# Optimization experiments

Measured on AMD Instinct MI355X. Metric: run time of the kernel, lower is better.

Reference implementation:

```python
import jax, jax.numpy as jnp
import numpy as np

H = 128      # hidden_channels
G = 512      # number of graphs in the batch
NEG_SLOPE = 0.2


def _seg_sum(x, idx, n):
    return jax.ops.segment_sum(x, idx, num_segments=n)


def _sage(x_src, x_dst, ei, Wl, bl, Wr):
    # PyG SAGEConv: lin_l(mean_j x_j) + lin_r(x_i); lin_l has bias, lin_r does not.
    s, d = ei[0], ei[1]
    n = x_dst.shape[0]
    agg = _seg_sum(x_src[s], d, n)
    cnt = _seg_sum(jnp.ones((ei.shape[1],), x_src.dtype), d, n)
    mean = agg / jnp.maximum(cnt, 1.0)[:, None]
    return mean @ Wl + bl + x_dst @ Wr


def _gat(x_src, x_dst, ei, Ws, Wd, a_s, a_d, b):
    # PyG GATConv (heads=1, add_self_loops=False, bipartite): segment softmax over dst.
    s, d = ei[0], ei[1]
    n = x_dst.shape[0]
    hs = x_src @ Ws                                  # [N_src, H]
    hd = x_dst @ Wd                                  # [N_dst, H]
    logit = jax.nn.leaky_relu((hs @ a_s)[s] + (hd @ a_d)[d], NEG_SLOPE)
    m = jax.ops.segment_max(logit, d, num_segments=n)
    e = jnp.exp(logit - m[d])
    z = _seg_sum(e, d, n)
    alpha = e / jnp.maximum(z[d], 1e-16)
    return _seg_sum(alpha[:, None] * hs[s], d, n) + b


def _gcn(x, ei, W, b):
    # PyG GCNConv with add_self_loops=True, normalize=True (same src/dst node type).
    s, d = ei[0], ei[1]
    n = x.shape[0]
    deg = _seg_sum(jnp.ones((ei.shape[1],), x.dtype), d, n) + 1.0  # +1 self loop
    dis = jax.lax.rsqrt(deg)
    h = x @ W
    norm = dis[s] * dis[d]
    out = _seg_sum(norm[:, None] * h[s], d, n) + (dis * dis)[:, None] * h
    return out + b


def _pool(x, b):
    s = _seg_sum(x, b, G)
    c = _seg_sum(jnp.ones((x.shape[0],), x.dtype), b, G)
    return s / jnp.maximum(c, 1.0)[:, None]


def setup_inputs() -> dict:
    key = jax.random.key(0)
    ks = iter(jax.random.split(key, 80))
    scale = 1.0 / np.sqrt(H)

    def nrm(shape, sc=scale):
        return jax.random.normal(next(ks), shape, jnp.float32) * sc

    def edges(e, n_src, n_dst):
        src = jax.random.randint(next(ks), (e,), 0, n_src, jnp.int32)
        dst = jax.random.randint(next(ks), (e,), 0, n_dst, jnp.int32)
        return jnp.stack([src, dst])

    def batch(n):
        return jnp.sort(jax.random.randint(next(ks), (n,), 0, G, jnp.int32))

    N_CD, N_SEQ, N_ANNO, N_RANGE, N_MD = 100000, 80000, 80000, 80000, 50000
    inp = {
        'x_cd': nrm((N_CD, H), 1.0), 'x_seq': nrm((N_SEQ, H), 1.0),
        'x_anno': nrm((N_ANNO, H), 1.0), 'x_range': nrm((N_RANGE, H), 1.0),
        'x_md': nrm((N_MD, H), 1.0),
        'ei_seq': edges(160000, N_CD, N_SEQ),
        'ei_anno': edges(200000, N_CD, N_ANNO),
        'ei_range': edges(200000, N_CD, N_RANGE),
        'ei_comp': edges(300000, N_MD, N_CD),
        'ei_cc': edges(300000, N_CD, N_CD),
        'ei_mm': edges(150000, N_MD, N_MD),
        'b_cd': batch(N_CD), 'b_seq': batch(N_SEQ), 'b_anno': batch(N_ANNO),
        'b_range': batch(N_RANGE), 'b_md': batch(N_MD),
    }
    # per-layer stacked params (leading axis = 2 layers)
    for nm, shp in [('Wsl_seq', (2, H, H)), ('bs_seq', (2, H)), ('Wsr_seq', (2, H, H)),
                    ('Wsl_anno', (2, H, H)), ('bs_anno', (2, H)), ('Wsr_anno', (2, H, H)),
                    ('Wg_comp_s', (2, H, H)), ('Wg_comp_d', (2, H, H)),
                    ('ag_comp_s', (2, H)), ('ag_comp_d', (2, H)), ('bg_comp', (2, H)),
                    ('Wg_range_s', (2, H, H)), ('Wg_range_d', (2, H, H)),
                    ('ag_range_s', (2, H)), ('ag_range_d', (2, H)), ('bg_range', (2, H)),
                    ('Wc_cc', (2, H, H)), ('bc_cc', (2, H)),
                    ('Wc_mm', (2, H, H)), ('bc_mm', (2, H)),
                    ('lin1_W', (5 * H, H)), ('lin1_b', (H,)),
                    ('lin2_W', (H, 1)), ('lin2_b', (1,))]:
        inp[nm] = nrm(shp)
    return inp


def reference(x_cd, x_seq, x_anno, x_range, x_md,
              ei_seq, ei_anno, ei_range, ei_comp, ei_cc, ei_mm,
              b_cd, b_seq, b_anno, b_range, b_md,
              Wsl_seq, bs_seq, Wsr_seq, Wsl_anno, bs_anno, Wsr_anno,
              Wg_comp_s, Wg_comp_d, ag_comp_s, ag_comp_d, bg_comp,
              Wg_range_s, Wg_range_d, ag_range_s, ag_range_d, bg_range,
              Wc_cc, bc_cc, Wc_mm, bc_mm,
              lin1_W, lin1_b, lin2_W, lin2_b):
    for l in range(2):
        # HeteroConv aggr='sum': CD receives GAT(MD->CD) + GCN(CD->CD)
        n_cd = (_gat(x_md, x_cd, ei_comp, Wg_comp_s[l], Wg_comp_d[l],
                     ag_comp_s[l], ag_comp_d[l], bg_comp[l])
                + _gcn(x_cd, ei_cc, Wc_cc[l], bc_cc[l]))
        n_seq = _sage(x_cd, x_seq, ei_seq, Wsl_seq[l], bs_seq[l], Wsr_seq[l])
        n_anno = _sage(x_cd, x_anno, ei_anno, Wsl_anno[l], bs_anno[l], Wsr_anno[l])
        n_range = _gat(x_cd, x_range, ei_range, Wg_range_s[l], Wg_range_d[l],
                       ag_range_s[l], ag_range_d[l], bg_range[l])
        n_md = _gcn(x_md, ei_mm, Wc_mm[l], bc_mm[l])
        x_cd, x_seq, x_anno, x_range, x_md = (
            jax.nn.relu(n_cd), jax.nn.relu(n_seq), jax.nn.relu(n_anno),
            jax.nn.relu(n_range), jax.nn.relu(n_md))
    emb = jnp.concatenate([_pool(x_cd, b_cd), _pool(x_seq, b_seq),
                           _pool(x_anno, b_anno), _pool(x_range, b_range),
                           _pool(x_md, b_md)], axis=-1)        # [G, 5H]
    h = jax.nn.relu(emb @ lin1_W + lin1_b)  # Dropout(0.7) is identity in eval
    return (h @ lin2_W + lin2_b).reshape(-1)  # [G]
```

## Files before the change

### kernel.cpp

```cpp
#include <hip/hip_runtime.h>

#define HD 128
#define GNUM 512
#define RPB 520
#define IDXCAP 512
#define TM 32

typedef __attribute__((ext_vector_type(8))) short short8v;
typedef __attribute__((ext_vector_type(4))) float f32x4;

__device__ __forceinline__ void split1(float a, short& h, short& l) {
  unsigned u = __float_as_uint(a);
  unsigned hb = (u + 0x7FFFu + ((u >> 16) & 1u)) & 0xFFFF0000u;
  h = (short)(hb >> 16);
  float rest = a - __uint_as_float(hb);
  unsigned u2 = __float_as_uint(rest);
  l = (short)((u2 + 0x7FFFu + ((u2 >> 16) & 1u)) >> 16);
}

struct WTab { const float* p[8]; };
__global__ __launch_bounds__(256) void k_split_w(WTab tab, short* __restrict__ whi,
                                                 short* __restrict__ wlo)
{
  int m = blockIdx.x >> 6;
  int i = (blockIdx.x & 63) * 256 + threadIdx.x;
  const float* W = tab.p[m >> 1] + (m & 1) * 16384;
  int k = i >> 7, n = i & 127;
  short h, l;
  split1(W[k * 128 + n], h, l);
  whi[m * 16384 + n * 128 + k] = h;
  wlo[m * 16384 + n * 128 + k] = l;
}

#define CF_LD 132
__global__ __launch_bounds__(256) void k_gemm_mfma(
    const float* __restrict__ A1, const short* __restrict__ WH1, const short* __restrict__ WL1,
    const int* __restrict__ grp, const int* __restrict__ gcol,
    const float* __restrict__ A2, const short* __restrict__ WH2, const short* __restrict__ WL2,
    float* __restrict__ C, const float* __restrict__ bias, int N, int relu,
    const float* __restrict__ avec, float* __restrict__ adot)
{
  __shared__ char smem[TM * 136 * 2 * 2];
  __shared__ int idxbuf[IDXCAP];
  short* Ah = (short*)smem;
  short* Al = Ah + TM * 136;
  float* Cf = (float*)smem;

  const int t = threadIdx.x;
  const int row0 = blockIdx.x * TM;
  const int lane = t & 63, wid = t >> 6;
  const int g = lane >> 4, cn = lane & 15;
  const int colbase = wid * 32;

  f32x4 zero = {0.f, 0.f, 0.f, 0.f};
  f32x4 acc[2][2];
#pragma unroll
  for (int rt = 0; rt < 2; ++rt) { acc[rt][0] = zero; acc[rt][1] = zero; }

  auto stageA = [&](const float* __restrict__ A) {
    const float4* A4 = (const float4*)(A + (size_t)row0 * 128);
#pragma unroll
    for (int i = 0; i < 4; ++i) {
      int f4 = t + i * 256;
      int row = f4 >> 5, c4 = f4 & 31;
      float4 v = make_float4(0.f, 0.f, 0.f, 0.f);
      if (row0 + row < N) v = A4[f4];
      short4 h, l;
      split1(v.x, h.x, l.x); split1(v.y, h.y, l.y);
      split1(v.z, h.z, l.z); split1(v.w, h.w, l.w);
      *(short4*)(Ah + row * 136 + c4 * 4) = h;
      *(short4*)(Al + row * 136 + c4 * 4) = l;
    }
  };

  auto stageA_gather = [&](const float* __restrict__ X, int e_lo) {
#pragma unroll
    for (int i = 0; i < 4; ++i) {
      int f4 = t + i * 256;
      int row = f4 >> 5, ln = f4 & 31;
      int r = row0 + row;
      float4 s = make_float4(0.f, 0.f, 0.f, 0.f);
      int e0 = 0, e1 = 0;
      if (r < N) { e0 = grp[r]; e1 = grp[r + 1]; }
      int e = e0;
      for (; e + 1 < e1; e += 2) {
        int off0 = e - e_lo, off1 = off0 + 1;
        int c0 = (off0 < IDXCAP) ? idxbuf[off0] : gcol[e];
        int c1 = (off1 < IDXCAP) ? idxbuf[off1] : gcol[e + 1];
        float4 v0 = *(const float4*)(X + (size_t)c0 * 128 + ln * 4);
        float4 v1 = *(const float4*)(X + (size_t)c1 * 128 + ln * 4);
        s.x += v0.x + v1.x; s.y += v0.y + v1.y;
        s.z += v0.z + v1.z; s.w += v0.w + v1.w;
      }
      if (e < e1) {
        int off = e - e_lo;
        int c = (off < IDXCAP) ? idxbuf[off] : gcol[e];
        float4 v = *(const float4*)(X + (size_t)c * 128 + ln * 4);
        s.x += v.x; s.y += v.y; s.z += v.z; s.w += v.w;
      }
      float inv = 1.f / fmaxf((float)(e1 - e0), 1.f);
      short4 h, l;
      split1(s.x * inv, h.x, l.x); split1(s.y * inv, h.y, l.y);
      split1(s.z * inv, h.z, l.z); split1(s.w * inv, h.w, l.w);
      *(short4*)(Ah + row * 136 + ln * 4) = h;
      *(short4*)(Al + row * 136 + ln * 4) = l;
    }
  };

  auto accum = [&](const short* __restrict__ WH, const short* __restrict__ WL) {
#pragma unroll
    for (int kg = 0; kg < 4; ++kg) {
      short8v bhi[2], blo[2];
#pragma unroll
      for (int ct = 0; ct < 2; ++ct) {
        size_t o = (size_t)(colbase + ct * 16 + cn) * 128 + kg * 32 + g * 8;
        bhi[ct] = *(const short8v*)(WH + o);
        blo[ct] = *(const short8v*)(WL + o);
      }
#pragma unroll
      for (int rt = 0; rt < 2; ++rt) {
        const int ao = (rt * 16 + cn) * 136 + kg * 32 + g * 8;
        const short8v ah = *(const short8v*)(Ah + ao);
        const short8v al = *(const short8v*)(Al + ao);
#pragma unroll
        for (int ct = 0; ct < 2; ++ct) {
          acc[rt][ct] = __builtin_amdgcn_mfma_f32_16x16x32_bf16(ah, bhi[ct], acc[rt][ct], 0, 0, 0);
          acc[rt][ct] = __builtin_amdgcn_mfma_f32_16x16x32_bf16(al, bhi[ct], acc[rt][ct], 0, 0, 0);
          acc[rt][ct] = __builtin_amdgcn_mfma_f32_16x16x32_bf16(ah, blo[ct], acc[rt][ct], 0, 0, 0);
        }
      }
    }
  };

  if (grp) {
    const int row_end = min(row0 + TM, N);
    const int e_lo = grp[row0];
    const int cnt = min(grp[row_end] - e_lo, IDXCAP);
    for (int k = t; k < cnt; k += 256) idxbuf[k] = gcol[e_lo + k];
    __syncthreads();
    stageA_gather(A1, e_lo);
  } else {
    stageA(A1);
  }
  __syncthreads();
  accum(WH1, WL1);
  if (A2) {
    __syncthreads();
    stageA(A2);
    __syncthreads();
    accum(WH2, WL2);
  }
  __syncthreads();

  if (avec) {
    float* part = (float*)smem;
    const float av0 = avec[colbase + cn];
    const float av1 = avec[colbase + 16 + cn];
#pragma unroll
    for (int rt = 0; rt < 2; ++rt)
#pragma unroll
      for (int r = 0; r < 4; ++r) {
        float p = fmaf(acc[rt][1][r], av1, acc[rt][0][r] * av0);
#pragma unroll
        for (int o = 1; o < 16; o <<= 1) p += __shfl_xor(p, o);
        if (cn == 0) part[wid * TM + rt * 16 + g * 4 + r] = p;
      }
    __syncthreads();
    if (t < TM) {
      int row = row0 + t;
      if (row < N) adot[row] = part[t] + part[TM + t] + part[2 * TM + t] + part[3 * TM + t];
    }
    __syncthreads();
  }

#pragma unroll
  for (int rt = 0; rt < 2; ++rt)
#pragma unroll
    for (int ct = 0; ct < 2; ++ct)
#pragma unroll
      for (int r = 0; r < 4; ++r)
        Cf[(rt * 16 + g * 4 + r) * CF_LD + colbase + ct * 16 + cn] = acc[rt][ct][r];
  __syncthreads();

  float4* C4 = (float4*)(C + (size_t)row0 * 128);
#pragma unroll
  for (int i = 0; i < 4; ++i) {
    int f4 = t + i * 256;
    int row = f4 >> 5, c4 = f4 & 31;
    if (row0 + row < N) {
      float4 v = *(const float4*)(Cf + row * CF_LD + c4 * 4);
      if (bias) {
        float4 bv = *(const float4*)(bias + c4 * 4);
        v.x += bv.x; v.y += bv.y; v.z += bv.z; v.w += bv.w;
      }
      if (relu) {
        v.x = fmaxf(v.x, 0.f); v.y = fmaxf(v.y, 0.f);
        v.z = fmaxf(v.z, 0.f); v.w = fmaxf(v.w, 0.f);
      }
      C4[f4] = v;
    }
  }
}

__global__ void k_rowdot(const float* __restrict__ x, const float* __restrict__ a,
                         float* __restrict__ out, int N)
{
  int wid = blockIdx.x * 4 + (threadIdx.x >> 6);
  int lane = threadIdx.x & 63;
  if (wid >= N) return;
  float2 xv = ((const float2*)x)[(size_t)wid * 64 + lane];
  float2 av = ((const float2*)a)[lane];
  float v = fmaf(xv.y, av.y, xv.x * av.x);
#pragma unroll
  for (int o = 32; o > 0; o >>= 1) v += __shfl_down(v, o);
  if (lane == 0) out[wid] = v;
}

struct MTab { const float* W[4]; const float* a[4]; };
__global__ __launch_bounds__(128) void k_matvec4(MTab tb, float* __restrict__ wv)
{
  __shared__ float as[128];
  int m = blockIdx.x, i = threadIdx.x;
  as[i] = tb.a[m][i];
  __syncthreads();
  const float* W = tb.W[m];
  float v = 0.f;
  for (int j = 0; j < 128; ++j) v = fmaf(W[i * 128 + j], as[j], v);
  wv[m * 128 + i] = v;
}

struct HTab { const int* key[6]; int* cnt[6]; unsigned short* rank[6]; int bo[7]; int n[6]; };
__global__ void k_hist_rank_all(HTab tb) {
  int bi = blockIdx.x, ty = 0;
  while (ty < 5 && bi >= tb.bo[ty + 1]) ++ty;
  int i = (bi - tb.bo[ty]) * 256 + threadIdx.x;
  if (i < tb.n[ty])
    tb.rank[ty][i] = (unsigned short)atomicAdd(&tb.cnt[ty][tb.key[ty][i]], 1);
}

struct FTab { const int* es[6]; const int* ed[6]; const int* rp[6];
              const unsigned short* rank[6]; int* col[6]; int bo[7]; int n[6]; };
__global__ void k_fill_all(FTab tb) {
  int bi = blockIdx.x, ty = 0;
  while (ty < 5 && bi >= tb.bo[ty + 1]) ++ty;
  int e = (bi - tb.bo[ty]) * 256 + threadIdx.x;
  if (e >= tb.n[ty]) return;
  int p = tb.rp[ty][tb.ed[ty][e]] + (int)tb.rank[ty][e];
  tb.col[ty][p] = tb.es[ty][e];
}

struct STab { int* rp[6]; int* bs[6]; int n[6]; int bo[7]; };

__global__ __launch_bounds__(256) void k_scan_partial_all(STab tb) {
  __shared__ int red[256];
  int bi = blockIdx.x, ty = 0;
  while (ty < 5 && bi >= tb.bo[ty + 1]) ++ty;
  int lb = bi - tb.bo[ty];
  const int* rp = tb.rp[ty];
  const int N = tb.n[ty];
  const int t = threadIdx.x, base = lb * 4096;
  int s = 0;
  for (int i = t; i < 4096; i += 256) {
    int idx = base + i;
    if (idx < N) s += rp[idx];
  }
  red[t] = s;
  __syncthreads();
  for (int ofs = 128; ofs > 0; ofs >>= 1) {
    if (t < ofs) red[t] += red[t + ofs];
    __syncthreads();
  }
  if (t == 0) tb.bs[ty][lb] = red[0];
}

__global__ __launch_bounds__(256) void k_scan_bsums_all(STab tb) {
  __shared__ int sh[256];
  const int ty = blockIdx.x;
  const int nb = (tb.n[ty] + 4095) / 4096;
  const int t = threadIdx.x;
  int v = (t < nb) ? tb.bs[ty][t] : 0;
  sh[t] = v;
  __syncthreads();
  for (int ofs = 1; ofs < 256; ofs <<= 1) {
    int u = (t >= ofs) ? sh[t - ofs] : 0;
    __syncthreads();
    sh[t] += u;
    __syncthreads();
  }
  if (t < nb) tb.bs[ty][t] = sh[t] - v;
  if (t == 255) tb.rp[ty][tb.n[ty]] = sh[255];
}

__global__ __launch_bounds__(256) void k_scan_final_all(STab tb) {
  __shared__ int sh[4096 + 256];
  __shared__ int tsum[256];
  int bi = blockIdx.x, ty = 0;
  while (ty < 5 && bi >= tb.bo[ty + 1]) ++ty;
  int lb = bi - tb.bo[ty];
  int* rp = tb.rp[ty];
  const int N = tb.n[ty];
  const int t = threadIdx.x, base = lb * 4096;
  auto mp = [](int i) { return i + (i >> 4); };
#pragma unroll
  for (int i = 0; i < 16; ++i) {
    int idx = base + i * 256 + t;
    sh[mp(i * 256 + t)] = (idx < N) ? rp[idx] : 0;
  }
  __syncthreads();
  int s = 0;
#pragma unroll
  for (int j = 0; j < 16; ++j) s += sh[mp(t * 16 + j)];
  tsum[t] = s;
  __syncthreads();
  for (int ofs = 1; ofs < 256; ofs <<= 1) {
    int u = (t >= ofs) ? tsum[t - ofs] : 0;
    __syncthreads();
    tsum[t] += u;
    __syncthreads();
  }
  int pre = tsum[t] - s + tb.bs[ty][lb];
#pragma unroll
  for (int j = 0; j < 16; ++j) {
    int v = sh[mp(t * 16 + j)];
    sh[mp(t * 16 + j)] = pre;
    pre += v;
  }
  __syncthreads();
#pragma unroll
  for (int i = 0; i < 16; ++i) {
    int idx = base + i * 256 + t;
    if (idx < N) rp[idx] = sh[mp(i * 256 + t)];
  }
}

struct BTab { const int* b[5]; int n[5]; };
__global__ __launch_bounds__(512) void k_runptr(BTab tb, int* __restrict__ rpb_all) {
  const int ty = blockIdx.x;
  const int* b = tb.b[ty];
  const int N = tb.n[ty];
  const int t = threadIdx.x;
  int lo = 0, hi = N;
  while (lo < hi) {
    int mid = (lo + hi) >> 1;
    if (b[mid] < t) lo = mid + 1; else hi = mid;
  }
  rpb_all[ty * RPB + t] = lo;
  if (t == 0) rpb_all[ty * RPB + GNUM] = N;
}

struct DTab { const int* rp[2]; float* dis[2]; int n[2]; int bo[3]; };
__global__ void k_dis2(DTab tb) {
  int bi = blockIdx.x, ty = (bi >= tb.bo[1]) ? 1 : 0;
  int n = (bi - tb.bo[ty]) * 256 + threadIdx.x;
  if (n < tb.n[ty]) tb.dis[ty][n] = rsqrtf((float)(tb.rp[ty][n + 1] - tb.rp[ty][n]) + 1.f);
}

__global__ void k_gcn_gather(const int* __restrict__ rp, const int* __restrict__ col,
                             const float* __restrict__ dis, const float* __restrict__ h,
                             const float* addin, const float* __restrict__ b,
                             float* out, int N,
                             const float* __restrict__ dvec, float* __restrict__ dout)
{
  int node = blockIdx.x * 4 + (threadIdx.x >> 6);
  if (node >= N) return;
  int lane = threadIdx.x & 63;
  int s0 = rp[node], deg = rp[node + 1] - s0;
  float rd = dis[node];
  const float2* h2 = (const float2*)h;
  float2 hself = h2[(size_t)node * 64 + lane];
  float2 bv = ((const float2*)b)[lane];
  float ad0 = 0.f, ad1 = 0.f;
  if (addin) {
    float2 a2 = ((const float2*)addin)[(size_t)node * 64 + lane];
    ad0 = a2.x; ad1 = a2.y;
  }
  float a0 = 0.f, a1 = 0.f, b0 = 0.f, b1 = 0.f;
  for (int base = 0; base < deg; base += 64) {
    int m = min(64, deg - base);
    int c = 0; float dv = 0.f;
    if (lane < m) { c = col[s0 + base + lane]; dv = dis[c]; }
    int j = 0;
    for (; j + 1 < m; j += 2) {
      int sA = __shfl(c, j), sB = __shfl(c, j + 1);
      float nA = __shfl(dv, j) * rd, nB = __shfl(dv, j + 1) * rd;
      float2 vA = h2[(size_t)sA * 64 + lane];
      float2 vB = h2[(size_t)sB * 64 + lane];
      a0 = fmaf(nA, vA.x, a0); a1 = fmaf(nA, vA.y, a1);
      b0 = fmaf(nB, vB.x, b0); b1 = fmaf(nB, vB.y, b1);
    }
    if (j < m) {
      int sA = __shfl(c, j);
      float nA = __shfl(dv, j) * rd;
      float2 vA = h2[(size_t)sA * 64 + lane];
      a0 = fmaf(nA, vA.x, a0); a1 = fmaf(nA, vA.y, a1);
    }
  }
  float rr = rd * rd;
  float v0 = fmaf(rr, hself.x, a0 + b0) + bv.x + ad0;
  float v1 = fmaf(rr, hself.y, a1 + b1) + bv.y + ad1;
  v0 = fmaxf(v0, 0.f); v1 = fmaxf(v1, 0.f);
  ((float2*)out)[(size_t)node * 64 + lane] = make_float2(v0, v1);
  if (dvec) {
    float2 wv = ((const float2*)dvec)[lane];
    float p = fmaf(v1, wv.y, v0 * wv.x);
#pragma unroll
    for (int o = 32; o > 0; o >>= 1) p += __shfl_xor(p, o);
    if (lane == 0) dout[node] = p;
  }
}

__global__ void k_gat_gather(const int* __restrict__ rp, const int* __restrict__ col,
                             const float* __restrict__ hs, const float* __restrict__ as_,
                             const float* __restrict__ ad_, const float* __restrict__ b,
                             float* __restrict__ out, int N, int relu,
                             const float* __restrict__ dvec, float* __restrict__ dout)
{
  int node = blockIdx.x * 4 + (threadIdx.x >> 6);
  if (node >= N) return;
  int lane = threadIdx.x & 63;
  int s0 = rp[node], deg = rp[node + 1] - s0;
  float adn = ad_[node];
  float2 bv = ((const float2*)b)[lane];
  const float2* hs2 = (const float2*)hs;
  float z = 0.f, a0 = 0.f, a1 = 0.f, b0 = 0.f, b1 = 0.f;
  for (int base = 0; base < deg; base += 64) {
    int m = min(64, deg - base);
    int c = 0; float av = 0.f;
    if (lane < m) { c = col[s0 + base + lane]; av = as_[c]; }
    int j = 0;
    for (; j + 1 < m; j += 2) {
      int sA = __shfl(c, j), sB = __shfl(c, j + 1);
      float vA = __shfl(av, j) + adn, vB = __shfl(av, j + 1) + adn;
      vA = vA > 0.f ? vA : 0.2f * vA;
      vB = vB > 0.f ? vB : 0.2f * vB;
      float pA = __expf(vA), pB = __expf(vB);
      z += pA + pB;
      float2 hA = hs2[(size_t)sA * 64 + lane];
      float2 hB = hs2[(size_t)sB * 64 + lane];
      a0 = fmaf(pA, hA.x, a0); a1 = fmaf(pA, hA.y, a1);
      b0 = fmaf(pB, hB.x, b0); b1 = fmaf(pB, hB.y, b1);
    }
    if (j < m) {
      int sA = __shfl(c, j);
      float vA = __shfl(av, j) + adn;
      vA = vA > 0.f ? vA : 0.2f * vA;
      float pA = __expf(vA);
      z += pA;
      float2 hA = hs2[(size_t)sA * 64 + lane];
      a0 = fmaf(pA, hA.x, a0); a1 = fmaf(pA, hA.y, a1);
    }
  }
  float inv = (deg > 0) ? 1.f / z : 0.f;
  float v0 = fmaf(a0 + b0, inv, bv.x);
  float v1 = fmaf(a1 + b1, inv, bv.y);
  if (relu) { v0 = fmaxf(v0, 0.f); v1 = fmaxf(v1, 0.f); }
  ((float2*)out)[(size_t)node * 64 + lane] = make_float2(v0, v1);
  if (dvec) {
    float2 wv = ((const float2*)dvec)[lane];
    float p = fmaf(v1, wv.y, v0 * wv.x);
#pragma unroll
    for (int o = 32; o > 0; o >>= 1) p += __shfl_xor(p, o);
    if (lane == 0) dout[node] = p;
  }
}

__global__ __launch_bounds__(256) void k_pool_seg(
    const float* __restrict__ x, const int* __restrict__ rpb,
    float* __restrict__ pool, int col_off)
{
  __shared__ float2 red2[4][64];
  const int g = blockIdx.x;
  const int t = threadIdx.x, w = t >> 6, lane = t & 63;
  const int n0 = rpb[g], n1 = rpb[g + 1];
  const float2* x2 = (const float2*)x;
  float a0 = 0.f, a1 = 0.f, b0 = 0.f, b1 = 0.f;
  int n = n0 + w;
  for (; n + 4 < n1; n += 8) {
    float2 vA = x2[(size_t)n * 64 + lane];
    float2 vB = x2[(size_t)(n + 4) * 64 + lane];
    a0 += vA.x; a1 += vA.y; b0 += vB.x; b1 += vB.y;
  }
  if (n < n1) { float2 vA = x2[(size_t)n * 64 + lane]; a0 += vA.x; a1 += vA.y; }
  red2[w][lane] = make_float2(a0 + b0, a1 + b1);
  __syncthreads();
  if (t < 64) {
    float2 r0 = red2[0][t], r1 = red2[1][t], r2 = red2[2][t], r3 = red2[3][t];
    float inv = 1.f / fmaxf((float)(n1 - n0), 1.f);
    ((float2*)(pool + (size_t)g * 640 + col_off))[t] =
        make_float2((r0.x + r1.x + r2.x + r3.x) * inv,
                    (r0.y + r1.y + r2.y + r3.y) * inv);
  }
}

__global__ void k_mlp(const float* __restrict__ pool,
                      const float* __restrict__ W1, const float* __restrict__ b1,
                      const float* __restrict__ W2, const float* __restrict__ b2,
                      float* __restrict__ out)
{
  __shared__ float emb[640];
  __shared__ float red[128];
  const int g = blockIdx.x, t = threadIdx.x;
  for (int i = t; i < 640; i += 128) emb[i] = pool[(size_t)g * 640 + i];
  __syncthreads();
  float acc = b1[t];
  for (int i = 0; i < 640; ++i) acc = fmaf(emb[i], W1[i * 128 + t], acc);
  float h = fmaxf(acc, 0.f);
  red[t] = h * W2[t];
  __syncthreads();
  for (int s = 64; s > 0; s >>= 1) {
    if (t < s) red[t] += red[t + s];
    __syncthreads();
  }
  if (t == 0) out[g] = red[0] + b2[0];
}

extern "C" void kernel_launch(void* const* d_in, const int* in_sizes, int n_in,
                              void* d_out, int out_size, void* d_ws, size_t ws_size,
                              hipStream_t stream)
{
  auto fin = [&](int i) { return (const float*)d_in[i]; };
  auto iin = [&](int i) { return (const int*)d_in[i]; };

  const float *x_cd = fin(0), *x_seq = fin(1), *x_anno = fin(2), *x_range = fin(3), *x_md = fin(4);
  const int *ei_seq = iin(5), *ei_anno = iin(6), *ei_range = iin(7),
            *ei_comp = iin(8), *ei_cc = iin(9), *ei_mm = iin(10);
  const int *b_cd = iin(11), *b_seq = iin(12), *b_anno = iin(13), *b_range = iin(14), *b_md = iin(15);

  const int N_CD = in_sizes[0] / HD, N_SEQ = in_sizes[1] / HD, N_ANNO = in_sizes[2] / HD,
            N_RANGE = in_sizes[3] / HD, N_MD = in_sizes[4] / HD;
  const int E_seq = in_sizes[5] / 2, E_anno = in_sizes[6] / 2, E_range = in_sizes[7] / 2,
            E_comp = in_sizes[8] / 2, E_cc = in_sizes[9] / 2, E_mm = in_sizes[10] / 2;
  const int N_OTH = max(max(N_SEQ, N_ANNO), N_RANGE);

  auto WLm = [&](int i, int l) { return fin(i) + (size_t)l * HD * HD; };
  auto WLv = [&](int i, int l) { return fin(i) + (size_t)l * HD; };

  float* ws = (float*)d_ws;
  size_t off = 0;
  auto alloc = [&](size_t n) { float* p = ws + off; off += (n + 3) & ~(size_t)3; return p; };
  float* xcd1 = alloc((size_t)N_CD * HD);
  float* xmd1 = alloc((size_t)N_MD * HD);
  float* xoth = alloc((size_t)N_OTH * HD);
  float* acc  = alloc((size_t)N_CD * HD);
  float* t1   = alloc((size_t)N_CD * HD);
  float* sAs  = alloc((size_t)N_CD);
  float* sAd  = alloc((size_t)N_CD);
  float* sAd2 = alloc((size_t)N_CD);
  float* dis_cc = alloc((size_t)N_CD);
  float* dis_mm = alloc((size_t)N_MD);
  float* wvall = alloc(4 * HD);
  float* pool = alloc((size_t)GNUM * 5 * HD);
  short* whi = (short*)(ws + off); off += (size_t)16 * 16384 / 2;
  short* wlo = (short*)(ws + off); off += (size_t)16 * 16384 / 2;
  auto alloci = [&](size_t n) { int* p = (int*)(ws + off); off += (n + 3) & ~(size_t)3; return p; };
  int* bsall = alloci(6 * 256);
  int* rpb_all = alloci(5 * RPB);
  int Nds[6] = {N_SEQ, N_ANNO, N_RANGE, N_CD, N_CD, N_MD};
  int Es[6]  = {E_seq, E_anno, E_range, E_comp, E_cc, E_mm};
  int* rps[6];
  int* rp0 = alloci(0);
  { size_t tot = 0; for (int i = 0; i < 6; ++i) tot += (size_t)Nds[i] + 1;
    int* p = alloci(tot); rp0 = p;
    for (int i = 0; i < 6; ++i) { rps[i] = p; p += Nds[i] + 1; } }
  size_t rp_tot_bytes = 0; for (int i = 0; i < 6; ++i) rp_tot_bytes += ((size_t)Nds[i] + 1) * 4;
  unsigned short* ranks[6];
  for (int i = 0; i < 6; ++i) ranks[i] = (unsigned short*)alloci(((size_t)Es[i] + 1) / 2);
  int* cols[6];  for (int i = 0; i < 6; ++i) cols[i] = alloci((size_t)Es[i]);
  (void)n_in;

  if (off * sizeof(float) > ws_size) {
    hipMemsetAsync(d_out, 0, (size_t)out_size * sizeof(float), stream);
    return;
  }

  auto ew = [&](size_t elems) { return dim3((unsigned)((elems + 255) / 256)); };
  auto nw = [&](int N) { return dim3((unsigned)((N + 3) / 4)); };

  WTab tab;
  tab.p[0] = fin(16); tab.p[1] = fin(18); tab.p[2] = fin(19); tab.p[3] = fin(21);
  tab.p[4] = fin(22); tab.p[5] = fin(27); tab.p[6] = fin(32); tab.p[7] = fin(34);
  k_split_w<<<dim3(1024), dim3(256), 0, stream>>>(tab, whi, wlo);

  MTab mt;
  mt.W[0] = WLm(23, 0); mt.a[0] = WLv(25, 0);
  mt.W[1] = WLm(23, 1); mt.a[1] = WLv(25, 1);
  mt.W[2] = WLm(28, 0); mt.a[2] = WLv(30, 0);
  mt.W[3] = WLm(28, 1); mt.a[3] = WLv(30, 1);
  k_matvec4<<<dim3(4), dim3(128), 0, stream>>>(mt, wvall);

  {
    BTab bt;
    bt.b[0] = b_cd; bt.n[0] = N_CD;  bt.b[1] = b_seq; bt.n[1] = N_SEQ;
    bt.b[2] = b_anno; bt.n[2] = N_ANNO;  bt.b[3] = b_range; bt.n[3] = N_RANGE;
    bt.b[4] = b_md; bt.n[4] = N_MD;
    k_runptr<<<dim3(5), dim3(512), 0, stream>>>(bt, rpb_all);
  }

  const int* ess[6] = {ei_seq, ei_anno, ei_range, ei_comp, ei_cc, ei_mm};
  const int* eds[6] = {ei_seq + E_seq, ei_anno + E_anno, ei_range + E_range,
                       ei_comp + E_comp, ei_cc + E_cc, ei_mm + E_mm};
  hipMemsetAsync(rp0, 0, rp_tot_bytes, stream);
  {
    HTab ht; int b = 0;
    for (int i = 0; i < 6; ++i) {
      ht.key[i] = eds[i]; ht.cnt[i] = rps[i]; ht.rank[i] = ranks[i];
      ht.bo[i] = b; b += (Es[i] + 255) / 256; ht.n[i] = Es[i];
    }
    ht.bo[6] = b;
    k_hist_rank_all<<<dim3(b), dim3(256), 0, stream>>>(ht);
  }
  {
    STab st; int b = 0;
    for (int i = 0; i < 6; ++i) {
      st.rp[i] = rps[i]; st.bs[i] = bsall + i * 256;
      st.n[i] = Nds[i]; st.bo[i] = b; b += (Nds[i] + 4095) / 4096;
    }
    st.bo[6] = b;
    k_scan_partial_all<<<dim3(b), dim3(256), 0, stream>>>(st);
    k_scan_bsums_all<<<dim3(6), dim3(256), 0, stream>>>(st);
    k_scan_final_all<<<dim3(b), dim3(256), 0, stream>>>(st);
  }
  {
    FTab ft; int b = 0;
    for (int i = 0; i < 6; ++i) {
      ft.es[i] = ess[i]; ft.ed[i] = eds[i]; ft.rp[i] = rps[i]; ft.rank[i] = ranks[i];
      ft.col[i] = cols[i]; ft.bo[i] = b; b += (Es[i] + 255) / 256; ft.n[i] = Es[i];
    }
    ft.bo[6] = b;
    k_fill_all<<<dim3(b), dim3(256), 0, stream>>>(ft);
  }
  int *rp_seq = rps[0], *rp_anno = rps[1], *rp_range = rps[2],
      *rp_comp = rps[3], *rp_cc = rps[4], *rp_mm = rps[5];
  int *col_seq = cols[0], *col_anno = cols[1], *col_range = cols[2],
      *col_comp = cols[3], *col_cc = cols[4], *col_mm = cols[5];
  {
    DTab dt;
    dt.rp[0] = rp_cc; dt.dis[0] = dis_cc; dt.n[0] = N_CD;
    dt.rp[1] = rp_mm; dt.dis[1] = dis_mm; dt.n[1] = N_MD;
    dt.bo[0] = 0; dt.bo[1] = (N_CD + 255) / 256;
    dt.bo[2] = dt.bo[1] + (N_MD + 255) / 256;
    k_dis2<<<dim3(dt.bo[2]), dim3(256), 0, stream>>>(dt);
  }

  auto WHp = [&](int sidx, int layer) { return whi + (size_t)(sidx * 2 + layer) * 16384; };
  auto WLp = [&](int sidx, int layer) { return wlo + (size_t)(sidx * 2 + layer) * 16384; };
  auto gemm = [&](const float* A, int sidx, int layer, float* C, const float* b,
                  int N, int relu, const float* avec = nullptr, float* adot = nullptr) {
    k_gemm_mfma<<<dim3((N + TM - 1) / TM), dim3(256), 0, stream>>>(
        A, WHp(sidx, layer), WLp(sidx, layer), nullptr, nullptr,
        nullptr, nullptr, nullptr, C, b, N, relu, avec, adot);
  };
  auto gemm2g = [&](const float* xsrc, const int* grp, const int* gcol, int s1,
                    const float* xself, int s2, int layer,
                    float* C, const float* b, int N) {
    k_gemm_mfma<<<dim3((N + TM - 1) / TM), dim3(256), 0, stream>>>(
        xsrc, WHp(s1, layer), WLp(s1, layer), grp, gcol,
        xself, WHp(s2, layer), WLp(s2, layer), C, b, N, 1, nullptr, nullptr);
  };
  auto do_pool = [&](const float* x, int type) {
    k_pool_seg<<<dim3(GNUM), dim3(256), 0, stream>>>(x, rpb_all + type * RPB, pool, type * HD);
  };

  auto gat = [&](const float* xs, const float* xd, const int* rp, const int* col,
                 int Ns, int Nd, int sidx, int layer, const float* avs_raw,
                 const float* sAd_src, int wvD,
                 const float* dvec, float* dout,
                 const float* bias, float* out, int relu) {
    if (wvD >= 0) {
      k_rowdot<<<nw(Nd), dim3(256), 0, stream>>>(xd, wvall + wvD * 128, sAd, Nd);
      sAd_src = sAd;
    }
    gemm(xs, sidx, layer, t1, nullptr, Ns, 0, avs_raw, sAs);
    k_gat_gather<<<nw(Nd), dim3(256), 0, stream>>>(rp, col, t1, sAs, sAd_src, bias,
                                                   out, Nd, relu, dvec, dout);
  };
  auto gcn = [&](const float* x, const int* rp, const int* col, const float* dis, int N,
                 int sidx, int layer, const float* b, const float* addin, float* out,
                 const float* dvec, float* dout) {
    gemm(x, sidx, layer, t1, nullptr, N, 0);
    k_gcn_gather<<<nw(N), dim3(256), 0, stream>>>(rp, col, dis, t1, addin, b, out, N,
                                                  dvec, dout);
  };
  auto sage = [&](const float* xsrc, const float* xself, const int* rp, const int* col,
                  int Nd, int sl, int sr, int layer, const float* bl, float* out) {
    gemm2g(xsrc, rp, col, sl, xself, sr, layer, out, bl, Nd);
  };

  gat(x_md, x_cd, rp_comp, col_comp, N_MD, N_CD, 4, 0, WLv(24, 0),
      nullptr, 0, nullptr, nullptr, WLv(26, 0), acc, 0);
  gcn(x_cd, rp_cc, col_cc, dis_cc, N_CD, 6, 0, WLv(33, 0), acc, xcd1,
      wvall + 1 * 128, sAd2);
  gcn(x_md, rp_mm, col_mm, dis_mm, N_MD, 7, 0, WLv(35, 0), nullptr, xmd1,
      nullptr, nullptr);
  gat(xmd1, xcd1, rp_comp, col_comp, N_MD, N_CD, 4, 1, WLv(24, 1),
      sAd2, -1, nullptr, nullptr, WLv(26, 1), acc, 0);
  gcn(xcd1, rp_cc, col_cc, dis_cc, N_CD, 6, 1, WLv(33, 1), acc, acc,
      nullptr, nullptr);
  do_pool(acc, 0);
  gcn(xmd1, rp_mm, col_mm, dis_mm, N_MD, 7, 1, WLv(35, 1), nullptr, acc,
      nullptr, nullptr);
  do_pool(acc, 4);

  sage(x_cd, x_seq, rp_seq, col_seq, N_SEQ, 0, 1, 0, WLv(17, 0), xoth);
  sage(xcd1, xoth, rp_seq, col_seq, N_SEQ, 0, 1, 1, WLv(17, 1), acc);
  do_pool(acc, 1);
  sage(x_cd, x_anno, rp_anno, col_anno, N_ANNO, 2, 3, 0, WLv(20, 0), xoth);
  sage(xcd1, xoth, rp_anno, col_anno, N_ANNO, 2, 3, 1, WLv(20, 1), acc);
  do_pool(acc, 2);
  gat(x_cd, x_range, rp_range, col_range, N_CD, N_RANGE, 5, 0, WLv(29, 0),
      nullptr, 2, wvall + 3 * 128, sAd2, WLv(31, 0), xoth, 1);
  gat(xcd1, xoth, rp_range, col_range, N_CD, N_RANGE, 5, 1, WLv(29, 1),
      sAd2, -1, nullptr, nullptr, WLv(31, 1), acc, 1);
  do_pool(acc, 3);

  k_mlp<<<dim3(GNUM), dim3(128), 0, stream>>>(
      pool, fin(36), fin(37), fin(38), fin(39), (float*)d_out);
}
```

Measured before the change: 988.0 us.

## Aggregate before transform: fuse GAT/GCN gathers into the MFMA GEMM prologue

Uses linearity to aggregate neighbour features first and then multiply by the weight, so GCN and GAT become a single gather-then-GEMM kernel instead of a GEMM into a temporary followed by a separate gather kernel. Attention logits are computed up front from precomputed W·a vectors via row dots and fused epilogue dot products, removing the intermediate h matrix write/read. The cost is that gathers now read raw inputs inside the GEMM staging, where the per-row work is imbalanced. Softmax also runs without max subtraction, as it did before.

```diff
diff --git a/kernel.cpp b/kernel.cpp
--- a/kernel.cpp
+++ b/kernel.cpp
@@ -33,15 +33,19 @@
 }
 
 #define CF_LD 132
-__global__ __launch_bounds__(256) void k_gemm_mfma(
+__global__ __launch_bounds__(256) void k_gemm_conv(
     const float* __restrict__ A1, const short* __restrict__ WH1, const short* __restrict__ WL1,
-    const int* __restrict__ grp, const int* __restrict__ gcol,
+    const int* __restrict__ grp, const int* __restrict__ gcol, int mode,
+    const float* __restrict__ wsrc, const float* __restrict__ rowsc,
     const float* __restrict__ A2, const short* __restrict__ WH2, const short* __restrict__ WL2,
-    float* __restrict__ C, const float* __restrict__ bias, int N, int relu,
-    const float* __restrict__ avec, float* __restrict__ adot)
+    float* __restrict__ C, const float* __restrict__ bias, const float* addin,
+    int N, int relu,
+    const float* __restrict__ avec, float* __restrict__ adot,
+    const float* __restrict__ avec2, float* __restrict__ adot2)
 {
   __shared__ char smem[TM * 136 * 2 * 2];
   __shared__ int idxbuf[IDXCAP];
+  __shared__ float wbuf[IDXCAP];
   short* Ah = (short*)smem;
   short* Al = Ah + TM * 136;
   float* Cf = (float*)smem;
@@ -57,6 +61,14 @@
 #pragma unroll
   for (int rt = 0; rt < 2; ++rt) { acc[rt][0] = zero; acc[rt][1] = zero; }
 
+  auto storeAhl = [&](int row, int ln, float4 s) {
+    short4 h, l;
+    split1(s.x, h.x, l.x); split1(s.y, h.y, l.y);
+    split1(s.z, h.z, l.z); split1(s.w, h.w, l.w);
+    *(short4*)(Ah + row * 136 + ln * 4) = h;
+    *(short4*)(Al + row * 136 + ln * 4) = l;
+  };
+
   auto stageA = [&](const float* __restrict__ A) {
     const float4* A4 = (const float4*)(A + (size_t)row0 * 128);
 #pragma unroll
@@ -65,15 +77,17 @@
       int row = f4 >> 5, c4 = f4 & 31;
       float4 v = make_float4(0.f, 0.f, 0.f, 0.f);
       if (row0 + row < N) v = A4[f4];
-      short4 h, l;
-      split1(v.x, h.x, l.x); split1(v.y, h.y, l.y);
-      split1(v.z, h.z, l.z); split1(v.w, h.w, l.w);
-      *(short4*)(Ah + row * 136 + c4 * 4) = h;
-      *(short4*)(Al + row * 136 + c4 * 4) = l;
+      storeAhl(row, c4, v);
     }
   };
 
-  auto stageA_gather = [&](const float* __restrict__ X, int e_lo) {
+  auto getcw = [&](int e, int e_lo, int& c, float& w) {
+    int off = e - e_lo;
+    if (off < IDXCAP) { c = idxbuf[off]; w = wbuf[off]; }
+    else { c = gcol[e]; w = wsrc ? wsrc[c] : 0.f; }
+  };
+
+  auto stage_gather = [&](const float* __restrict__ X, int e_lo) {
 #pragma unroll
     for (int i = 0; i < 4; ++i) {
       int f4 = t + i * 256;
@@ -81,29 +95,54 @@
       int r = row0 + row;
       float4 s = make_float4(0.f, 0.f, 0.f, 0.f);
       int e0 = 0, e1 = 0;
-      if (r < N) { e0 = grp[r]; e1 = grp[r + 1]; }
+      float rs = 0.f;
+      if (r < N) {
+        e0 = grp[r]; e1 = grp[r + 1];
+        if (mode >= 2) rs = rowsc[r];
+      }
+      float z = 0.f;
+      if (mode == 2 && r < N) {
+        float4 xs_ = *(const float4*)(X + (size_t)r * 128 + ln * 4);
+        float rr = rs * rs;
+        s.x = rr * xs_.x; s.y = rr * xs_.y; s.z = rr * xs_.z; s.w = rr * xs_.w;
+      }
       int e = e0;
       for (; e + 1 < e1; e += 2) {
-        int off0 = e - e_lo, off1 = off0 + 1;
-        int c0 = (off0 < IDXCAP) ? idxbuf[off0] : gcol[e];
-        int c1 = (off1 < IDXCAP) ? idxbuf[off1] : gcol[e + 1];
-        float4 v0 = *(const float4*)(X + (size_t)c0 * 128 + ln * 4);
-        float4 v1 = *(const float4*)(X + (size_t)c1 * 128 + ln * 4);
-        s.x += v0.x + v1.x; s.y += v0.y + v1.y;
-        s.z += v0.z + v1.z; s.w += v0.w + v1.w;
+        int c0, c1; float w0, w1;
+        getcw(e, e_lo, c0, w0);
+        getcw(e + 1, e_lo, c1, w1);
+        float p0, p1;
+        if (mode == 3) {
+          float v0 = w0 + rs; v0 = v0 > 0.f ? v0 : 0.2f * v0;
+          float v1 = w1 + rs; v1 = v1 > 0.f ? v1 : 0.2f * v1;
+          p0 = __expf(v0); p1 = __expf(v1); z += p0 + p1;
+        } else if (mode == 2) { p0 = w0 * rs; p1 = w1 * rs; }
+        else { p0 = 1.f; p1 = 1.f; }
+        float4 a = *(const float4*)(X + (size_t)c0 * 128 + ln * 4);
+        float4 b = *(const float4*)(X + (size_t)c1 * 128 + ln * 4);
+        s.x += p0 * a.x + p1 * b.x; s.y += p0 * a.y + p1 * b.y;
+        s.z += p0 * a.z + p1 * b.z; s.w += p0 * a.w + p1 * b.w;
       }
       if (e < e1) {
-        int off = e - e_lo;
-        int c = (off < IDXCAP) ? idxbuf[off] : gcol[e];
-        float4 v = *(const float4*)(X + (size_t)c * 128 + ln * 4);
-        s.x += v.x; s.y += v.y; s.z += v.z; s.w += v.w;
-      }
-      float inv = 1.f / fmaxf((float)(e1 - e0), 1.f);
-      short4 h, l;
-      split1(s.x * inv, h.x, l.x); split1(s.y * inv, h.y, l.y);
-      split1(s.z * inv, h.z, l.z); split1(s.w * inv, h.w, l.w);
-      *(short4*)(Ah + row * 136 + ln * 4) = h;
-      *(short4*)(Al + row * 136 + ln * 4) = l;
+        int c; float w;
+        getcw(e, e_lo, c, w);
+        float p;
+        if (mode == 3) {
+          float v = w + rs; v = v > 0.f ? v : 0.2f * v;
+          p = __expf(v); z += p;
+        } else if (mode == 2) p = w * rs;
+        else p = 1.f;
+        float4 a = *(const float4*)(X + (size_t)c * 128 + ln * 4);
+        s.x += p * a.x; s.y += p * a.y; s.z += p * a.z; s.w += p * a.w;
+      }
+      if (mode == 1) {
+        float inv = 1.f / fmaxf((float)(e1 - e0), 1.f);
+        s.x *= inv; s.y *= inv; s.z *= inv; s.w *= inv;
+      } else if (mode == 3) {
+        float inv = (e1 > e0) ? 1.f / z : 0.f;
+        s.x *= inv; s.y *= inv; s.z *= inv; s.w *= inv;
+      }
+      storeAhl(row, ln, s);
     }
   };
 
@@ -132,13 +171,17 @@
     }
   };
 
-  if (grp) {
+  if (mode != 0) {
     const int row_end = min(row0 + TM, N);
     const int e_lo = grp[row0];
     const int cnt = min(grp[row_end] - e_lo, IDXCAP);
-    for (int k = t; k < cnt; k += 256) idxbuf[k] = gcol[e_lo + k];
-    __syncthreads();
-    stageA_gather(A1, e_lo);
+    for (int k = t; k < cnt; k += 256) {
+      int idx = gcol[e_lo + k];
+      idxbuf[k] = idx;
+      if (wsrc) wbuf[k] = wsrc[idx];
+    }
+    __syncthreads();
+    stage_gather(A1, e_lo);
   } else {
     stageA(A1);
   }
@@ -151,27 +194,6 @@
     accum(WH2, WL2);
   }
   __syncthreads();
-
-  if (avec) {
-    float* part = (float*)smem;
-    const float av0 = avec[colbase + cn];
-    const float av1 = avec[colbase + 16 + cn];
-#pragma unroll
-    for (int rt = 0; rt < 2; ++rt)
-#pragma unroll
-      for (int r = 0; r < 4; ++r) {
-        float p = fmaf(acc[rt][1][r], av1, acc[rt][0][r] * av0);
-#pragma unroll
-        for (int o = 1; o < 16; o <<= 1) p += __shfl_xor(p, o);
-        if (cn == 0) part[wid * TM + rt * 16 + g * 4 + r] = p;
-      }
-    __syncthreads();
-    if (t < TM) {
-      int row = row0 + t;
-      if (row < N) adot[row] = part[t] + part[TM + t] + part[2 * TM + t] + part[3 * TM + t];
-    }
-    __syncthreads();
-  }
 
 #pragma unroll
   for (int rt = 0; rt < 2; ++rt)
@@ -193,11 +215,29 @@
         float4 bv = *(const float4*)(bias + c4 * 4);
         v.x += bv.x; v.y += bv.y; v.z += bv.z; v.w += bv.w;
       }
+      if (addin) {
+        float4 av = *(const float4*)(addin + (size_t)(row0 + row) * 128 + c4 * 4);
+        v.x += av.x; v.y += av.y; v.z += av.z; v.w += av.w;
+      }
       if (relu) {
         v.x = fmaxf(v.x, 0.f); v.y = fmaxf(v.y, 0.f);
         v.z = fmaxf(v.z, 0.f); v.w = fmaxf(v.w, 0.f);
       }
       C4[f4] = v;
+      if (avec) {
+        float4 av = *(const float4*)(avec + c4 * 4);
+        float p = v.x * av.x + v.y * av.y + v.z * av.z + v.w * av.w;
+#pragma unroll
+        for (int o = 1; o < 32; o <<= 1) p += __shfl_xor(p, o);
+        if (c4 == 0) adot[row0 + row] = p;
+      }
+      if (avec2) {
+        float4 av = *(const float4*)(avec2 + c4 * 4);
+        float p = v.x * av.x + v.y * av.y + v.z * av.z + v.w * av.w;
+#pragma unroll
+        for (int o = 1; o < 32; o <<= 1) p += __shfl_xor(p, o);
+        if (c4 == 0) adot2[row0 + row] = p;
+      }
     }
   }
 }
@@ -216,8 +256,25 @@
   if (lane == 0) out[wid] = v;
 }
 
-struct MTab { const float* W[4]; const float* a[4]; };
-__global__ __launch_bounds__(128) void k_matvec4(MTab tb, float* __restrict__ wv)
+__global__ void k_rowdot2(const float* __restrict__ x, const float* __restrict__ a1,
+                          const float* __restrict__ a2, float* __restrict__ o1,
+                          float* __restrict__ o2, int N)
+{
+  int wid = blockIdx.x * 4 + (threadIdx.x >> 6);
+  int lane = threadIdx.x & 63;
+  if (wid >= N) return;
+  float2 xv = ((const float2*)x)[(size_t)wid * 64 + lane];
+  float2 av1 = ((const float2*)a1)[lane];
+  float2 av2 = ((const float2*)a2)[lane];
+  float v1 = fmaf(xv.y, av1.y, xv.x * av1.x);
+  float v2 = fmaf(xv.y, av2.y, xv.x * av2.x);
+#pragma unroll
+  for (int o = 32; o > 0; o >>= 1) { v1 += __shfl_down(v1, o); v2 += __shfl_down(v2, o); }
+  if (lane == 0) { o1[wid] = v1; o2[wid] = v2; }
+}
+
+struct MTab { const float* W[8]; const float* a[8]; };
+__global__ __launch_bounds__(128) void k_matvec8(MTab tb, float* __restrict__ wv)
 {
   __shared__ float as[128];
   int m = blockIdx.x, i = threadIdx.x;
@@ -355,115 +412,6 @@
   if (n < tb.n[ty]) tb.dis[ty][n] = rsqrtf((float)(tb.rp[ty][n + 1] - tb.rp[ty][n]) + 1.f);
 }
 
-__global__ void k_gcn_gather(const int* __restrict__ rp, const int* __restrict__ col,
-                             const float* __restrict__ dis, const float* __restrict__ h,
-                             const float* addin, const float* __restrict__ b,
-                             float* out, int N,
-                             const float* __restrict__ dvec, float* __restrict__ dout)
-{
-  int node = blockIdx.x * 4 + (threadIdx.x >> 6);
-  if (node >= N) return;
-  int lane = threadIdx.x & 63;
-  int s0 = rp[node], deg = rp[node + 1] - s0;
-  float rd = dis[node];
-  const float2* h2 = (const float2*)h;
-  float2 hself = h2[(size_t)node * 64 + lane];
-  float2 bv = ((const float2*)b)[lane];
-  float ad0 = 0.f, ad1 = 0.f;
-  if (addin) {
-    float2 a2 = ((const float2*)addin)[(size_t)node * 64 + lane];
-    ad0 = a2.x; ad1 = a2.y;
-  }
-  float a0 = 0.f, a1 = 0.f, b0 = 0.f, b1 = 0.f;
-  for (int base = 0; base < deg; base += 64) {
-    int m = min(64, deg - base);
-    int c = 0; float dv = 0.f;
-    if (lane < m) { c = col[s0 + base + lane]; dv = dis[c]; }
-    int j = 0;
-    for (; j + 1 < m; j += 2) {
-      int sA = __shfl(c, j), sB = __shfl(c, j + 1);
-      float nA = __shfl(dv, j) * rd, nB = __shfl(dv, j + 1) * rd;
-      float2 vA = h2[(size_t)sA * 64 + lane];
-      float2 vB = h2[(size_t)sB * 64 + lane];
-      a0 = fmaf(nA, vA.x, a0); a1 = fmaf(nA, vA.y, a1);
-      b0 = fmaf(nB, vB.x, b0); b1 = fmaf(nB, vB.y, b1);
-    }
-    if (j < m) {
-      int sA = __shfl(c, j);
-      float nA = __shfl(dv, j) * rd;
-      float2 vA = h2[(size_t)sA * 64 + lane];
-      a0 = fmaf(nA, vA.x, a0); a1 = fmaf(nA, vA.y, a1);
-    }
-  }
-  float rr = rd * rd;
-  float v0 = fmaf(rr, hself.x, a0 + b0) + bv.x + ad0;
-  float v1 = fmaf(rr, hself.y, a1 + b1) + bv.y + ad1;
-  v0 = fmaxf(v0, 0.f); v1 = fmaxf(v1, 0.f);
-  ((float2*)out)[(size_t)node * 64 + lane] = make_float2(v0, v1);
-  if (dvec) {
-    float2 wv = ((const float2*)dvec)[lane];
-    float p = fmaf(v1, wv.y, v0 * wv.x);
-#pragma unroll
-    for (int o = 32; o > 0; o >>= 1) p += __shfl_xor(p, o);
-    if (lane == 0) dout[node] = p;
-  }
-}
-
-__global__ void k_gat_gather(const int* __restrict__ rp, const int* __restrict__ col,
-                             const float* __restrict__ hs, const float* __restrict__ as_,
-                             const float* __restrict__ ad_, const float* __restrict__ b,
-                             float* __restrict__ out, int N, int relu,
-                             const float* __restrict__ dvec, float* __restrict__ dout)
-{
-  int node = blockIdx.x * 4 + (threadIdx.x >> 6);
-  if (node >= N) return;
-  int lane = threadIdx.x & 63;
-  int s0 = rp[node], deg = rp[node + 1] - s0;
-  float adn = ad_[node];
-  float2 bv = ((const float2*)b)[lane];
-  const float2* hs2 = (const float2*)hs;
-  float z = 0.f, a0 = 0.f, a1 = 0.f, b0 = 0.f, b1 = 0.f;
-  for (int base = 0; base < deg; base += 64) {
-    int m = min(64, deg - base);
-    int c = 0; float av = 0.f;
-    if (lane < m) { c = col[s0 + base + lane]; av = as_[c]; }
-    int j = 0;
-    for (; j + 1 < m; j += 2) {
-      int sA = __shfl(c, j), sB = __shfl(c, j + 1);
-      float vA = __shfl(av, j) + adn, vB = __shfl(av, j + 1) + adn;
-      vA = vA > 0.f ? vA : 0.2f * vA;
-      vB = vB > 0.f ? vB : 0.2f * vB;
-      float pA = __expf(vA), pB = __expf(vB);
-      z += pA + pB;
-      float2 hA = hs2[(size_t)sA * 64 + lane];
-      float2 hB = hs2[(size_t)sB * 64 + lane];
-      a0 = fmaf(pA, hA.x, a0); a1 = fmaf(pA, hA.y, a1);
-      b0 = fmaf(pB, hB.x, b0); b1 = fmaf(pB, hB.y, b1);
-    }
-    if (j < m) {
-      int sA = __shfl(c, j);
-      float vA = __shfl(av, j) + adn;
-      vA = vA > 0.f ? vA : 0.2f * vA;
-      float pA = __expf(vA);
-      z += pA;
-      float2 hA = hs2[(size_t)sA * 64 + lane];
-      a0 = fmaf(pA, hA.x, a0); a1 = fmaf(pA, hA.y, a1);
-    }
-  }
-  float inv = (deg > 0) ? 1.f / z : 0.f;
-  float v0 = fmaf(a0 + b0, inv, bv.x);
-  float v1 = fmaf(a1 + b1, inv, bv.y);
-  if (relu) { v0 = fmaxf(v0, 0.f); v1 = fmaxf(v1, 0.f); }
-  ((float2*)out)[(size_t)node * 64 + lane] = make_float2(v0, v1);
-  if (dvec) {
-    float2 wv = ((const float2*)dvec)[lane];
-    float p = fmaf(v1, wv.y, v0 * wv.x);
-#pragma unroll
-    for (int o = 32; o > 0; o >>= 1) p += __shfl_xor(p, o);
-    if (lane == 0) dout[node] = p;
-  }
-}
-
 __global__ __launch_bounds__(256) void k_pool_seg(
     const float* __restrict__ x, const int* __restrict__ rpb,
     float* __restrict__ pool, int col_off)
@@ -543,12 +491,15 @@
   float* xoth = alloc((size_t)N_OTH * HD);
   float* acc  = alloc((size_t)N_CD * HD);
   float* t1   = alloc((size_t)N_CD * HD);
-  float* sAs  = alloc((size_t)N_CD);
-  float* sAd  = alloc((size_t)N_CD);
-  float* sAd2 = alloc((size_t)N_CD);
+  float* sA = alloc((size_t)N_CD);
+  float* sB = alloc((size_t)N_CD);
+  float* sC = alloc((size_t)N_CD);
+  float* sD = alloc((size_t)N_CD);
+  float* sE = alloc((size_t)N_CD);
+  float* sF = alloc((size_t)N_CD);
   float* dis_cc = alloc((size_t)N_CD);
   float* dis_mm = alloc((size_t)N_MD);
-  float* wvall = alloc(4 * HD);
+  float* wv8 = alloc(8 * HD);
   float* pool = alloc((size_t)GNUM * 5 * HD);
   short* whi = (short*)(ws + off); off += (size_t)16 * 16384 / 2;
   short* wlo = (short*)(ws + off); off += (size_t)16 * 16384 / 2;
@@ -582,11 +533,20 @@
   k_split_w<<<dim3(1024), dim3(256), 0, stream>>>(tab, whi, wlo);
 
   MTab mt;
-  mt.W[0] = WLm(23, 0); mt.a[0] = WLv(25, 0);
-  mt.W[1] = WLm(23, 1); mt.a[1] = WLv(25, 1);
-  mt.W[2] = WLm(28, 0); mt.a[2] = WLv(30, 0);
-  mt.W[3] = WLm(28, 1); mt.a[3] = WLv(30, 1);
-  k_matvec4<<<dim3(4), dim3(128), 0, stream>>>(mt, wvall);
+  mt.W[0] = WLm(22, 0); mt.a[0] = WLv(24, 0);
+  mt.W[1] = WLm(23, 0); mt.a[1] = WLv(25, 0);
+  mt.W[2] = WLm(22, 1); mt.a[2] = WLv(24, 1);
+  mt.W[3] = WLm(23, 1); mt.a[3] = WLv(25, 1);
+  mt.W[4] = WLm(27, 0); mt.a[4] = WLv(29, 0);
+  mt.W[5] = WLm(28, 0); mt.a[5] = WLv(30, 0);
+  mt.W[6] = WLm(27, 1); mt.a[6] = WLv(29, 1);
+  mt.W[7] = WLm(28, 1); mt.a[7] = WLv(30, 1);
+  k_matvec8<<<dim3(8), dim3(128), 0, stream>>>(mt, wv8);
+
+  k_rowdot<<<nw(N_MD), dim3(256), 0, stream>>>(x_md, wv8 + 0 * 128, sA, N_MD);
+  k_rowdot2<<<nw(N_CD), dim3(256), 0, stream>>>(x_cd, wv8 + 1 * 128, wv8 + 4 * 128,
+                                                sB, sC, N_CD);
+  k_rowdot<<<nw(N_RANGE), dim3(256), 0, stream>>>(x_range, wv8 + 5 * 128, sD, N_RANGE);
 
   {
     BTab bt;
@@ -644,73 +604,51 @@
 
   auto WHp = [&](int sidx, int layer) { return whi + (size_t)(sidx * 2 + layer) * 16384; };
   auto WLp = [&](int sidx, int layer) { return wlo + (size_t)(sidx * 2 + layer) * 16384; };
-  auto gemm = [&](const float* A, int sidx, int layer, float* C, const float* b,
-                  int N, int relu, const float* avec = nullptr, float* adot = nullptr) {
-    k_gemm_mfma<<<dim3((N + TM - 1) / TM), dim3(256), 0, stream>>>(
-        A, WHp(sidx, layer), WLp(sidx, layer), nullptr, nullptr,
-        nullptr, nullptr, nullptr, C, b, N, relu, avec, adot);
-  };
-  auto gemm2g = [&](const float* xsrc, const int* grp, const int* gcol, int s1,
-                    const float* xself, int s2, int layer,
-                    float* C, const float* b, int N) {
-    k_gemm_mfma<<<dim3((N + TM - 1) / TM), dim3(256), 0, stream>>>(
-        xsrc, WHp(s1, layer), WLp(s1, layer), grp, gcol,
-        xself, WHp(s2, layer), WLp(s2, layer), C, b, N, 1, nullptr, nullptr);
+
+  auto conv = [&](int mode, const float* A1, int sidx, int layer,
+                  const int* grp, const int* gcol,
+                  const float* wsrc, const float* rowsc,
+                  const float* A2, int sidx2,
+                  float* C, const float* bias, const float* addin, int N, int relu,
+                  const float* avec, float* adot, const float* avec2, float* adot2) {
+    k_gemm_conv<<<dim3((N + TM - 1) / TM), dim3(256), 0, stream>>>(
+        A1, WHp(sidx, layer), WLp(sidx, layer), grp, gcol, mode, wsrc, rowsc,
+        A2, A2 ? WHp(sidx2, layer) : nullptr, A2 ? WLp(sidx2, layer) : nullptr,
+        C, bias, addin, N, relu, avec, adot, avec2, adot2);
   };
   auto do_pool = [&](const float* x, int type) {
     k_pool_seg<<<dim3(GNUM), dim3(256), 0, stream>>>(x, rpb_all + type * RPB, pool, type * HD);
   };
 
-  auto gat = [&](const float* xs, const float* xd, const int* rp, const int* col,
-                 int Ns, int Nd, int sidx, int layer, const float* avs_raw,
-                 const float* sAd_src, int wvD,
-                 const float* dvec, float* dout,
-                 const float* bias, float* out, int relu) {
-    if (wvD >= 0) {
-      k_rowdot<<<nw(Nd), dim3(256), 0, stream>>>(xd, wvall + wvD * 128, sAd, Nd);
-      sAd_src = sAd;
-    }
-    gemm(xs, sidx, layer, t1, nullptr, Ns, 0, avs_raw, sAs);
-    k_gat_gather<<<nw(Nd), dim3(256), 0, stream>>>(rp, col, t1, sAs, sAd_src, bias,
-                                                   out, Nd, relu, dvec, dout);
-  };
-  auto gcn = [&](const float* x, const int* rp, const int* col, const float* dis, int N,
-                 int sidx, int layer, const float* b, const float* addin, float* out,
-                 const float* dvec, float* dout) {
-    gemm(x, sidx, layer, t1, nullptr, N, 0);
-    k_gcn_gather<<<nw(N), dim3(256), 0, stream>>>(rp, col, dis, t1, addin, b, out, N,
-                                                  dvec, dout);
-  };
-  auto sage = [&](const float* xsrc, const float* xself, const int* rp, const int* col,
-                  int Nd, int sl, int sr, int layer, const float* bl, float* out) {
-    gemm2g(xsrc, rp, col, sl, xself, sr, layer, out, bl, Nd);
-  };
-
-  gat(x_md, x_cd, rp_comp, col_comp, N_MD, N_CD, 4, 0, WLv(24, 0),
-      nullptr, 0, nullptr, nullptr, WLv(26, 0), acc, 0);
-  gcn(x_cd, rp_cc, col_cc, dis_cc, N_CD, 6, 0, WLv(33, 0), acc, xcd1,
-      wvall + 1 * 128, sAd2);
-  gcn(x_md, rp_mm, col_mm, dis_mm, N_MD, 7, 0, WLv(35, 0), nullptr, xmd1,
-      nullptr, nullptr);
-  gat(xmd1, xcd1, rp_comp, col_comp, N_MD, N_CD, 4, 1, WLv(24, 1),
-      sAd2, -1, nullptr, nullptr, WLv(26, 1), acc, 0);
-  gcn(xcd1, rp_cc, col_cc, dis_cc, N_CD, 6, 1, WLv(33, 1), acc, acc,
-      nullptr, nullptr);
+  conv(3, x_md, 4, 0, rp_comp, col_comp, sA, sB, nullptr, 0,
+       acc, WLv(26, 0), nullptr, N_CD, 0, nullptr, nullptr, nullptr, nullptr);
+  conv(2, x_cd, 6, 0, rp_cc, col_cc, dis_cc, dis_cc, nullptr, 0,
+       xcd1, WLv(33, 0), acc, N_CD, 1, wv8 + 3 * 128, sB, wv8 + 6 * 128, sE);
+  conv(2, x_md, 7, 0, rp_mm, col_mm, dis_mm, dis_mm, nullptr, 0,
+       xmd1, WLv(35, 0), nullptr, N_MD, 1, wv8 + 2 * 128, sA, nullptr, nullptr);
+  conv(3, xmd1, 4, 1, rp_comp, col_comp, sA, sB, nullptr, 0,
+       acc, WLv(26, 1), nullptr, N_CD, 0, nullptr, nullptr, nullptr, nullptr);
+  conv(2, xcd1, 6, 1, rp_cc, col_cc, dis_cc, dis_cc, nullptr, 0,
+       acc, WLv(33, 1), acc, N_CD, 1, nullptr, nullptr, nullptr, nullptr);
   do_pool(acc, 0);
-  gcn(xmd1, rp_mm, col_mm, dis_mm, N_MD, 7, 1, WLv(35, 1), nullptr, acc,
-      nullptr, nullptr);
+  conv(2, xmd1, 7, 1, rp_mm, col_mm, dis_mm, dis_mm, nullptr, 0,
+       acc, WLv(35, 1), nullptr, N_MD, 1, nullptr, nullptr, nullptr, nullptr);
   do_pool(acc, 4);
 
-  sage(x_cd, x_seq, rp_seq, col_seq, N_SEQ, 0, 1, 0, WLv(17, 0), xoth);
-  sage(xcd1, xoth, rp_seq, col_seq, N_SEQ, 0, 1, 1, WLv(17, 1), acc);
+  conv(1, x_cd, 0, 0, rp_seq, col_seq, nullptr, nullptr, x_seq, 1,
+       xoth, WLv(17, 0), nullptr, N_SEQ, 1, nullptr, nullptr, nullptr, nullptr);
+  conv(1, xcd1, 0, 1, rp_seq, col_seq, nullptr, nullptr, xoth, 1,
+       acc, WLv(17, 1), nullptr, N_SEQ, 1, nullptr, nullptr, nullptr, nullptr);
   do_pool(acc, 1);
-  sage(x_cd, x_anno, rp_anno, col_anno, N_ANNO, 2, 3, 0, WLv(20, 0), xoth);
-  sage(xcd1, xoth, rp_anno, col_anno, N_ANNO, 2, 3, 1, WLv(20, 1), acc);
+  conv(1, x_cd, 2, 0, rp_anno, col_anno, nullptr, nullptr, x_anno, 3,
+       t1, WLv(20, 0), nullptr, N_ANNO, 1, nullptr, nullptr, nullptr, nullptr);
+  conv(1, xcd1, 2, 1, rp_anno, col_anno, nullptr, nullptr, t1, 3,
+       acc, WLv(20, 1), nullptr, N_ANNO, 1, nullptr, nullptr, nullptr, nullptr);
   do_pool(acc, 2);
-  gat(x_cd, x_range, rp_range, col_range, N_CD, N_RANGE, 5, 0, WLv(29, 0),
-      nullptr, 2, wvall + 3 * 128, sAd2, WLv(31, 0), xoth, 1);
-  gat(xcd1, xoth, rp_range, col_range, N_CD, N_RANGE, 5, 1, WLv(29, 1),
-      sAd2, -1, nullptr, nullptr, WLv(31, 1), acc, 1);
+  conv(3, x_cd, 5, 0, rp_range, col_range, sC, sD, nullptr, 0,
+       xoth, WLv(31, 0), nullptr, N_RANGE, 1, wv8 + 7 * 128, sF, nullptr, nullptr);
+  conv(3, xcd1, 5, 1, rp_range, col_range, sE, sF, nullptr, 0,
+       acc, WLv(31, 1), nullptr, N_RANGE, 1, nullptr, nullptr, nullptr, nullptr);
   do_pool(acc, 3);
 
   k_mlp<<<dim3(GNUM), dim3(128), 0, stream>>>(
```

New measurement: 923.7 us. -6.5%, faster.
